# Kernel tuning notes

Hardware: AMD Instinct MI355X
Metric: run time of the kernel (lower is better)

## Reference

```python
import jax, jax.numpy as jnp
import numpy as np

ALPHA = 0.9

def setup_inputs() -> dict:
    key = jax.random.key(0)
    inputs = jax.random.normal(key, (16, 4000, 512), dtype=jnp.float32)
    return {"inputs": inputs}

def reference(inputs) -> jnp.ndarray:
    # y_t = (1-alpha) * y_{t-1} + alpha * x_t, with y_{-1} = 0
    # (matches torch loop: y_0 = alpha * x_0)
    a = jnp.asarray(ALPHA, dtype=inputs.dtype)
    one_minus_a = jnp.asarray(1.0 - ALPHA, dtype=inputs.dtype)
    x_t = jnp.swapaxes(inputs, 0, 1)  # [T, B, C] for scan over time

    def step(carry, x):
        y = one_minus_a * carry + a * x
        return y, y

    init = jnp.zeros(x_t.shape[1:], dtype=inputs.dtype)  # [B, C]
    _, ys = jax.lax.scan(step, init, x_t)  # ys: [T, B, C]
    return jnp.swapaxes(ys, 0, 1)  # [B, T, C]
```

## Files before the change

### kernel.cpp

```cpp
#include <hip/hip_runtime.h>


constexpr int B_ = 16;
constexpr int T_ = 4000;
constexpr int C_ = 512;
constexpr int L_ = 8;
constexpr int W_ = 8;
constexpr int NC4_ = C_ / 4;
constexpr int NCHUNK_ = T_ / L_;

__global__ __launch_bounds__(256, 4) void ema_chunk_scan(const float* __restrict__ x,
                                                         float* __restrict__ y) {
    int g = blockIdx.x * blockDim.x + threadIdx.x;
    int c4 = g & (NC4_ - 1);
    int bt = g >> 7;
    int b  = bt & (B_ - 1);
    int chunk = bt >> 4;

    int t0 = chunk * L_;
    int tw = (chunk > 0) ? (t0 - W_) : 0;

    const float4* pw = (const float4*)(x + ((size_t)b * T_ + tw) * C_) + c4;
    const float4* pm = (const float4*)(x + ((size_t)b * T_ + t0) * C_) + c4;
    float4*       q  = (float4*)(y + ((size_t)b * T_ + t0) * C_) + c4;

    float4 w[W_];
    #pragma unroll
    for (int i = 0; i < W_; ++i) w[i] = pw[(size_t)i * NC4_];
    float4 m[L_];
    #pragma unroll
    for (int i = 0; i < L_; ++i) m[i] = pm[(size_t)i * NC4_];

    const float a = 0.9f, om = 0.1f;
    float4 acc = make_float4(0.f, 0.f, 0.f, 0.f);

    #pragma unroll
    for (int i = 0; i < W_; ++i) {
        acc.x = om * acc.x + a * w[i].x;
        acc.y = om * acc.y + a * w[i].y;
        acc.z = om * acc.z + a * w[i].z;
        acc.w = om * acc.w + a * w[i].w;
    }
    float sel = (chunk > 0) ? 1.f : 0.f;
    acc.x *= sel; acc.y *= sel; acc.z *= sel; acc.w *= sel;

    #pragma unroll
    for (int i = 0; i < L_; ++i) {
        acc.x = om * acc.x + a * m[i].x;
        acc.y = om * acc.y + a * m[i].y;
        acc.z = om * acc.z + a * m[i].z;
        acc.w = om * acc.w + a * m[i].w;
        q[(size_t)i * NC4_] = acc;
    }
}

extern "C" void kernel_launch(void* const* d_in, const int* in_sizes, int n_in,
                              void* d_out, int out_size, void* d_ws, size_t ws_size,
                              hipStream_t stream) {
    const float* x = (const float*)d_in[0];
    float* y = (float*)d_out;
    int total_threads = B_ * NC4_ * NCHUNK_;
    int block = 256;
    int grid = total_threads / block;
    ema_chunk_scan<<<grid, block, 0, stream>>>(x, y);
}
```

Measured before the change: 229.9 us.

## Lengthen scan chunks, software-pipeline chunk loads, and use nontemporal stores

Raises the time-chunk length from 8 to 32 while keeping an 8-step warmup window. Each thread now reads 40 input rows to produce 32 outputs, instead of 16 rows for 8, which cuts redundant input reads. The 32-step chunk is processed as two 16-row halves: loads for the second half are issued while the first half is being computed, keeping register pressure bounded. Outputs are written with nontemporal stores to avoid polluting the cache. The trade-off is a quarter as many threads and more live registers per thread, which may reduce latency hiding.

```diff
diff --git a/kernel.cpp b/kernel.cpp
--- a/kernel.cpp
+++ b/kernel.cpp
@@ -4,10 +4,19 @@
 constexpr int B_ = 16;
 constexpr int T_ = 4000;
 constexpr int C_ = 512;
-constexpr int L_ = 8;
+constexpr int L_ = 32;
 constexpr int W_ = 8;
+constexpr int BL_ = 16;
 constexpr int NC4_ = C_ / 4;
 constexpr int NCHUNK_ = T_ / L_;
+
+typedef float f32x4_ __attribute__((ext_vector_type(4)));
+
+__device__ __forceinline__ void nt_store4(float4* p, const float4& v) {
+    f32x4_ t;
+    t.x = v.x; t.y = v.y; t.z = v.z; t.w = v.w;
+    __builtin_nontemporal_store(t, (f32x4_*)p);
+}
 
 __global__ __launch_bounds__(256, 4) void ema_chunk_scan(const float* __restrict__ x,
                                                          float* __restrict__ y) {
@@ -20,16 +29,15 @@
     int t0 = chunk * L_;
     int tw = (chunk > 0) ? (t0 - W_) : 0;
 
-    const float4* pw = (const float4*)(x + ((size_t)b * T_ + tw) * C_) + c4;
-    const float4* pm = (const float4*)(x + ((size_t)b * T_ + t0) * C_) + c4;
-    float4*       q  = (float4*)(y + ((size_t)b * T_ + t0) * C_) + c4;
+    const float4* base = (const float4*)(x + (size_t)b * T_ * C_) + c4;
+    float4*       q    = (float4*)(y + ((size_t)b * T_ + t0) * C_) + c4;
 
     float4 w[W_];
     #pragma unroll
-    for (int i = 0; i < W_; ++i) w[i] = pw[(size_t)i * NC4_];
-    float4 m[L_];
+    for (int i = 0; i < W_; ++i) w[i] = base[(size_t)(tw + i) * NC4_];
+    float4 m[BL_];
     #pragma unroll
-    for (int i = 0; i < L_; ++i) m[i] = pm[(size_t)i * NC4_];
+    for (int i = 0; i < BL_; ++i) m[i] = base[(size_t)(t0 + i) * NC4_];
 
     const float a = 0.9f, om = 0.1f;
     float4 acc = make_float4(0.f, 0.f, 0.f, 0.f);
@@ -45,12 +53,22 @@
     acc.x *= sel; acc.y *= sel; acc.z *= sel; acc.w *= sel;
 
     #pragma unroll
-    for (int i = 0; i < L_; ++i) {
+    for (int i = 0; i < BL_; ++i) {
+        float4 v = m[i];
+        m[i] = base[(size_t)(t0 + BL_ + i) * NC4_];
+        acc.x = om * acc.x + a * v.x;
+        acc.y = om * acc.y + a * v.y;
+        acc.z = om * acc.z + a * v.z;
+        acc.w = om * acc.w + a * v.w;
+        nt_store4(&q[(size_t)i * NC4_], acc);
+    }
+    #pragma unroll
+    for (int i = 0; i < BL_; ++i) {
         acc.x = om * acc.x + a * m[i].x;
         acc.y = om * acc.y + a * m[i].y;
         acc.z = om * acc.z + a * m[i].z;
         acc.w = om * acc.w + a * m[i].w;
-        q[(size_t)i * NC4_] = acc;
+        nt_store4(&q[(size_t)(BL_ + i) * NC4_], acc);
     }
 }
 
```

Measured after the change: 233.4 us. No clear change (+1.5%).
